# Kernel optimization log

Measured on AMD Instinct MI355X. Metric: run time of the kernel, lower is better.

## Reference

```python
import jax, jax.numpy as jnp
import numpy as np


def setup_inputs() -> dict:
    key = jax.random.key(0)
    ks = jax.random.split(key, 5)
    B, T, D, H = 64, 512, 512, 1024
    s_ih = 1.0 / np.sqrt(D)
    s_hh = 1.0 / np.sqrt(H)
    return {
        "x": jax.random.normal(ks[0], (B, T, D), dtype=jnp.float32),
        "W_ih": jax.random.normal(ks[1], (4 * H, D), dtype=jnp.float32) * s_ih,
        "b_ih": jax.random.normal(ks[2], (4 * H,), dtype=jnp.float32) * s_ih,
        "W_hh": jax.random.normal(ks[3], (4 * H, H), dtype=jnp.float32) * s_hh,
        "b_hh": jax.random.normal(ks[4], (4 * H,), dtype=jnp.float32) * s_hh,
    }


def _lstm(x, W_ih, b_ih, W_hh, b_hh):
    B, T, D = x.shape
    H = W_hh.shape[1]
    # Precompute input-side gate projections for all timesteps at once: [B, T, 4H]
    gates_x = jnp.einsum("btd,gd->btg", x, W_ih) + b_ih + b_hh

    def step(carry, gx_t):
        h, c = carry
        g = gx_t + h @ W_hh.T  # [B, 4H]
        i, f, gc, o = jnp.split(g, 4, axis=-1)  # torch gate order: i, f, g, o
        i = jax.nn.sigmoid(i)
        f = jax.nn.sigmoid(f)
        gc = jnp.tanh(gc)
        o = jax.nn.sigmoid(o)
        c_new = f * c + i * gc
        h_new = o * jnp.tanh(c_new)
        return (h_new, c_new), h_new

    h0 = jnp.zeros((B, H), dtype=x.dtype)
    c0 = jnp.zeros((B, H), dtype=x.dtype)
    (h_last, c_last), hs = jax.lax.scan(step, (h0, c0), jnp.swapaxes(gates_x, 0, 1))
    output = jnp.swapaxes(hs, 0, 1)  # [B, T, H]
    return output, (h_last, c_last)


def reference(x, W_ih, b_ih, W_hh, b_hh):
    return _lstm(x, W_ih, b_ih, W_hh, b_hh)
```

## Files before the change

kernel.cpp:

```cpp
#include <hip/hip_runtime.h>


typedef __attribute__((ext_vector_type(4))) float f32x4;
typedef __attribute__((ext_vector_type(4))) unsigned u32x4;
typedef __attribute__((ext_vector_type(8))) __bf16 bf16x8;
typedef __attribute__((ext_vector_type(4))) __bf16 bf16x4;

__device__ __forceinline__ f32x4 mfma16(bf16x8 a, bf16x8 b, f32x4 c) {
  return __builtin_amdgcn_mfma_f32_16x16x32_bf16(a, b, c, 0, 0, 0);
}
__device__ __forceinline__ float sigm(float x) {
  return __builtin_amdgcn_rcpf(1.0f + __expf(-x));
}
__device__ __forceinline__ float tanh_(float x) {
  return 2.0f * __builtin_amdgcn_rcpf(1.0f + __expf(-2.0f * x)) - 1.0f;
}
__device__ __forceinline__ unsigned umin2(unsigned a, unsigned b) { return a < b ? a : b; }

template<bool GF32>
__global__ __launch_bounds__(256) void k_gates(
    const float* __restrict__ x, const float* __restrict__ Wih,
    const float* __restrict__ bih, const float* __restrict__ bhh,
    void* __restrict__ gates)
{
  __shared__ __align__(16) __bf16 lA[128][40];
  __shared__ __align__(16) __bf16 lB[128][40];
  int bid = blockIdx.x;
  int grp = bid >> 9;
  int rem = bid & 511;
  int mt = rem & 31;
  int nt = (grp << 4) + (rem >> 5);
  const int m0 = mt << 7, n0 = nt << 7;
  const int tid = threadIdx.x, lane = tid & 63, wave = tid >> 6;
  const int cl = lane & 15, rg = lane >> 4;
  const int wm = (wave >> 1) << 6, wn = (wave & 1) << 6;
  f32x4 acc[4][4] = {};

  const int r = tid >> 1;
  const int kh = (tid & 1) << 4;
  const float* aSrc = Wih + (size_t)(m0 + r) * 512 + kh;
  const int nn = n0 + r;
  const float* bSrc = x + ((size_t)(nn & 63) * 512 + (nn >> 6)) * 512 + kh;

  for (int k0 = 0; k0 < 512; k0 += 32) {
    __syncthreads();
    #pragma unroll
    for (int i = 0; i < 16; i += 4) {
      f32x4 va = *(const f32x4*)(aSrc + k0 + i);
      f32x4 vb = *(const f32x4*)(bSrc + k0 + i);
      bf16x4 pa, pb;
      #pragma unroll
      for (int j = 0; j < 4; ++j) { pa[j] = (__bf16)va[j]; pb[j] = (__bf16)vb[j]; }
      *(bf16x4*)&lA[r][kh + i] = pa;
      *(bf16x4*)&lB[r][kh + i] = pb;
    }
    __syncthreads();
    bf16x8 afr[4], bfr[4];
    #pragma unroll
    for (int q = 0; q < 4; ++q) {
      afr[q] = *(const bf16x8*)&lA[wm + q * 16 + cl][rg * 8];
      bfr[q] = *(const bf16x8*)&lB[wn + q * 16 + cl][rg * 8];
    }
    #pragma unroll
    for (int mi = 0; mi < 4; ++mi)
      #pragma unroll
      for (int ni = 0; ni < 4; ++ni)
        acc[mi][ni] = mfma16(afr[mi], bfr[ni], acc[mi][ni]);
  }

  #pragma unroll
  for (int mi = 0; mi < 4; ++mi) {
    int gb = m0 + wm + mi * 16 + rg * 4;
    f32x4 bsum = *(const f32x4*)(bih + gb);
    bsum += *(const f32x4*)(bhh + gb);
    #pragma unroll
    for (int ni = 0; ni < 4; ++ni) {
      int n = n0 + wn + ni * 16 + cl;
      int tt = n >> 6, bb = n & 63;
      #pragma unroll
      for (int v = 0; v < 4; ++v) {
        float val = acc[mi][ni][v] + bsum[v];
        size_t idx = ((size_t)tt * 4096 + (size_t)(gb + v)) * 64 + bb;
        if (GF32) ((float*)gates)[idx] = val;
        else      ((__bf16*)gates)[idx] = (__bf16)val;
      }
    }
  }
}

template<bool GF32>
__global__ __launch_bounds__(256, 1) void k_rnn(
    const void* __restrict__ gates, const float* __restrict__ Whh,
    __bf16* __restrict__ hA, __bf16* __restrict__ hB,
    unsigned* __restrict__ tags,
    float* __restrict__ out, float* __restrict__ hlast, float* __restrict__ clast)
{
  __shared__ __align__(16) __bf16 WF[2 * 32 * 64 * 8];
  const int tid = threadIdx.x, lane = tid & 63, wave = tid >> 6;
  const int cl = lane & 15, rg = lane >> 4;
  const int hb = blockIdx.x << 3;
  const int bo = wave << 4;
  const int bb = bo + rg * 4;
  const int wid = (blockIdx.x << 2) + wave;

  int wrowA[2];
  #pragma unroll
  for (int nt = 0; nt < 2; ++nt) {
    int nl = nt * 16 + cl;
    wrowA[nt] = (nl >> 3) * 1024 + hb + (nl & 7);
  }

  if (wave == 0) {
    #pragma unroll
    for (int nt = 0; nt < 2; ++nt) {
      const float* wsrc = Whh + (size_t)wrowA[nt] * 1024 + rg * 8;
      for (int kt = 0; kt < 32; ++kt) {
        f32x4 lo = *(const f32x4*)(wsrc + kt * 32);
        f32x4 hi = *(const f32x4*)(wsrc + kt * 32 + 4);
        bf16x8 f;
        #pragma unroll
        for (int j = 0; j < 4; ++j) { f[j] = (__bf16)lo[j]; f[4 + j] = (__bf16)hi[j]; }
        *(bf16x8*)&WF[(((size_t)nt * 32 + kt) * 64 + lane) * 8] = f;
      }
    }
  }
  __syncthreads();

  float cst[4] = {0.f, 0.f, 0.f, 0.f};
  float hvp[4] = {0.f, 0.f, 0.f, 0.f};

  f32x4 gp[2];
  #pragma unroll
  for (int nt = 0; nt < 2; ++nt) {
    size_t idx = (size_t)wrowA[nt] * 64 + bb;
    if (GF32) gp[nt] = *(const f32x4*)((const float*)gates + idx);
    else {
      bf16x4 q = *(const bf16x4*)((const __bf16*)gates + idx);
      #pragma unroll
      for (int j = 0; j < 4; ++j) gp[nt][j] = (float)q[j];
    }
  }

  for (int t = 0; t < 512; ++t) {
    if (t) {
      const unsigned* tp = tags + (lane << 3);
      for (;;) {
        u32x4 ta, tb;
        asm volatile(
          "global_load_dwordx4 %0, %2, off sc0 sc1\n\t"
          "global_load_dwordx4 %1, %2, off offset:16 sc0 sc1"
          : "=v"(ta), "=v"(tb) : "v"(tp) : "memory");
        asm volatile("s_waitcnt vmcnt(0)" ::: "memory");
        __builtin_amdgcn_sched_barrier(0);
        unsigned m = umin2(umin2(umin2(ta[0], ta[1]), umin2(ta[2], ta[3])),
                           umin2(umin2(tb[0], tb[1]), umin2(tb[2], tb[3])));
        if (__all((int)(m >= (unsigned)t))) break;
        __builtin_amdgcn_s_sleep(1);
      }
    }

    f32x4 acc0 = gp[0], acc1 = gp[1];

    bf16x8 af[32];
    if (t) {
      const __bf16* hsrc = (t & 1) ? hB : hA;
      const __bf16* hrow = hsrc + (size_t)(bo + cl) * 1024 + rg * 8;
      #pragma unroll
      for (int kt = 0; kt < 32; ++kt)
        asm volatile("global_load_dwordx4 %0, %1, off offset:%2 sc0 sc1"
                     : "=v"(af[kt]) : "v"(hrow), "i"(kt * 64) : "memory");
    }
    __builtin_amdgcn_sched_barrier(0);

    if (t && cl < 8) {
      #pragma unroll
      for (int v = 0; v < 4; ++v)
        __builtin_nontemporal_store(
            hvp[v], &out[((size_t)(bb + v) * 512 + (t - 1)) * 1024 + hb + cl]);
    }
    {
      int tn = (t < 511) ? t + 1 : t;
      #pragma unroll
      for (int nt = 0; nt < 2; ++nt) {
        size_t idx = ((size_t)tn * 4096 + (size_t)wrowA[nt]) * 64 + bb;
        if (GF32) gp[nt] = *(const f32x4*)((const float*)gates + idx);
        else {
          bf16x4 q = *(const bf16x4*)((const __bf16*)gates + idx);
          #pragma unroll
          for (int j = 0; j < 4; ++j) gp[nt][j] = (float)q[j];
        }
      }
    }
    __builtin_amdgcn_sched_barrier(0);

    if (t) {
      asm volatile("s_waitcnt vmcnt(20)" ::: "memory");
      __builtin_amdgcn_sched_barrier(0);
      #pragma unroll
      for (int kt = 0; kt < 16; ++kt) {
        acc0 = mfma16(af[kt], *(const bf16x8*)&WF[((size_t)kt * 64 + lane) * 8], acc0);
        acc1 = mfma16(af[kt], *(const bf16x8*)&WF[((size_t)(32 + kt) * 64 + lane) * 8], acc1);
      }
      asm volatile("s_waitcnt vmcnt(6)" ::: "memory");
      __builtin_amdgcn_sched_barrier(0);
      #pragma unroll
      for (int kt = 16; kt < 32; ++kt) {
        acc0 = mfma16(af[kt], *(const bf16x8*)&WF[((size_t)kt * 64 + lane) * 8], acc0);
        acc1 = mfma16(af[kt], *(const bf16x8*)&WF[((size_t)(32 + kt) * 64 + lane) * 8], acc1);
      }
    }

    f32x4 a0s, a1s;
    #pragma unroll
    for (int j = 0; j < 4; ++j) {
      a0s[j] = __shfl_xor(acc0[j], 8, 64);
      a1s[j] = __shfl_xor(acc1[j], 8, 64);
    }
    float hv[4];
    #pragma unroll
    for (int v = 0; v < 4; ++v) {
      float iv = sigm(acc0[v]);
      float fv = sigm(a0s[v]);
      float gv = tanh_(acc1[v]);
      float ov = sigm(a1s[v]);
      float c = fv * cst[v] + iv * gv;
      cst[v] = c;
      hv[v] = ov * tanh_(c);
    }

    __bf16* hnext = (t & 1) ? hA : hB;
    #pragma unroll
    for (int v = 0; v < 4; ++v) {
      union { __bf16 b; unsigned short s; } cvt;
      cvt.b = (__bf16)hv[v];
      int me = cvt.s;
      int nb = __shfl_xor(me, 1, 64);
      if (cl < 8 && (cl & 1) == 0) {
        unsigned word = (unsigned)(me & 0xffff) | ((unsigned)(nb & 0xffff) << 16);
        unsigned* p = (unsigned*)hnext + (((size_t)(bb + v)) << 9) + ((hb + cl) >> 1);
        asm volatile("global_store_dword %0, %1, off sc0 sc1"
                     :: "v"(p), "v"(word) : "memory");
      }
    }
    asm volatile("s_waitcnt vmcnt(0)" ::: "memory");
    if (lane == 0 && t < 511) {
      unsigned tv = (unsigned)(t + 1);
      unsigned* tp = tags + wid;
      asm volatile("global_store_dword %0, %1, off sc0 sc1"
                   :: "v"(tp), "v"(tv) : "memory");
    }

    #pragma unroll
    for (int v = 0; v < 4; ++v) hvp[v] = hv[v];
  }

  if (cl < 8) {
    #pragma unroll
    for (int v = 0; v < 4; ++v) {
      int b = bb + v;
      __builtin_nontemporal_store(hvp[v], &out[((size_t)b * 512 + 511) * 1024 + hb + cl]);
      __builtin_nontemporal_store(hvp[v], &hlast[(size_t)b * 1024 + hb + cl]);
      __builtin_nontemporal_store(cst[v], &clast[(size_t)b * 1024 + hb + cl]);
    }
  }
}

extern "C" void kernel_launch(void* const* d_in, const int* in_sizes, int n_in,
                              void* d_out, int out_size, void* d_ws, size_t ws_size,
                              hipStream_t stream) {
  const float* x   = (const float*)d_in[0];
  const float* Wih = (const float*)d_in[1];
  const float* bih = (const float*)d_in[2];
  const float* Whh = (const float*)d_in[3];
  const float* bhh = (const float*)d_in[4];
  float* out   = (float*)d_out;
  float* hlast = out + (size_t)64 * 512 * 1024;
  float* clast = hlast + (size_t)64 * 1024;

  char* ws = (char*)d_ws;
  unsigned* tags = (unsigned*)ws;
  __bf16* hA = (__bf16*)(ws + 4096);
  __bf16* hB = (__bf16*)(ws + 4096 + 131072);
  void* gates = (void*)(ws + (1 << 20));
  const size_t need_f32 = (size_t)(1 << 20) + (size_t)512 * 4096 * 64 * 4;
  bool gf32 = (ws_size >= need_f32);

  hipMemsetAsync(tags, 0, 2048, stream);

  if (gf32) {
    k_gates<true><<<8192, 256, 0, stream>>>(x, Wih, bih, bhh, gates);
    k_rnn<true><<<128, 256, 0, stream>>>(gates, Whh, hA, hB, tags, out, hlast, clast);
  } else {
    k_gates<false><<<8192, 256, 0, stream>>>(x, Wih, bih, bhh, gates);
    k_rnn<false><<<128, 256, 0, stream>>>(gates, Whh, hA, hB, tags, out, hlast, clast);
  }
}
```

Baseline: 3.838 ms.

## Use per-block tags with barrier instead of per-wave tags in LSTM recurrence

Each block now synchronizes its four waves with __syncthreads and publishes a single progress tag, so pollers read 128 tags (two per lane, one dwordx2 load) instead of 512 tags (eight per lane). This reduces global polling traffic and the min-reduction per spin. In exchange, every block pays an intra-block barrier each step, and a block's tag advances only when its slowest wave finishes. Output stores also change from nontemporal builtins to plain global stores, and the memset size and a WF index expression are rewritten.

```diff
diff --git a/kernel.cpp b/kernel.cpp
--- a/kernel.cpp
+++ b/kernel.cpp
@@ -2,7 +2,7 @@
 
 
 typedef __attribute__((ext_vector_type(4))) float f32x4;
-typedef __attribute__((ext_vector_type(4))) unsigned u32x4;
+typedef __attribute__((ext_vector_type(2))) unsigned u32x2;
 typedef __attribute__((ext_vector_type(8))) __bf16 bf16x8;
 typedef __attribute__((ext_vector_type(4))) __bf16 bf16x4;
 
@@ -100,8 +100,7 @@
   const int cl = lane & 15, rg = lane >> 4;
   const int hb = blockIdx.x << 3;
   const int bo = wave << 4;
-  const int bb = bo + rg * 4;
-  const int wid = (blockIdx.x << 2) + wave;
+  const int bb = bo + (rg << 2);
 
   int wrowA[2];
   #pragma unroll
@@ -143,17 +142,14 @@
 
   for (int t = 0; t < 512; ++t) {
     if (t) {
-      const unsigned* tp = tags + (lane << 3);
+      const unsigned* tp = tags + (lane << 1);
       for (;;) {
-        u32x4 ta, tb;
-        asm volatile(
-          "global_load_dwordx4 %0, %2, off sc0 sc1\n\t"
-          "global_load_dwordx4 %1, %2, off offset:16 sc0 sc1"
-          : "=v"(ta), "=v"(tb) : "v"(tp) : "memory");
+        u32x2 ta;
+        asm volatile("global_load_dwordx2 %0, %1, off sc0 sc1"
+                     : "=v"(ta) : "v"(tp) : "memory");
         asm volatile("s_waitcnt vmcnt(0)" ::: "memory");
         __builtin_amdgcn_sched_barrier(0);
-        unsigned m = umin2(umin2(umin2(ta[0], ta[1]), umin2(ta[2], ta[3])),
-                           umin2(umin2(tb[0], tb[1]), umin2(tb[2], tb[3])));
+        unsigned m = umin2(ta[0], ta[1]);
         if (__all((int)(m >= (unsigned)t))) break;
         __builtin_amdgcn_s_sleep(1);
       }
@@ -174,9 +170,10 @@
 
     if (t && cl < 8) {
       #pragma unroll
-      for (int v = 0; v < 4; ++v)
-        __builtin_nontemporal_store(
-            hvp[v], &out[((size_t)(bb + v) * 512 + (t - 1)) * 1024 + hb + cl]);
+      for (int v = 0; v < 4; ++v) {
+        float* p = &out[((size_t)(bb + v) * 512 + (t - 1)) * 1024 + hb + cl];
+        asm volatile("global_store_dword %0, %1, off" :: "v"(p), "v"(hvp[v]) : "memory");
+      }
     }
     {
       int tn = (t < 511) ? t + 1 : t;
@@ -206,7 +203,7 @@
       #pragma unroll
       for (int kt = 16; kt < 32; ++kt) {
         acc0 = mfma16(af[kt], *(const bf16x8*)&WF[((size_t)kt * 64 + lane) * 8], acc0);
-        acc1 = mfma16(af[kt], *(const bf16x8*)&WF[((size_t)(32 + kt) * 64 + lane) * 8], acc1);
+        acc1 = mfma16(af[kt], *(const bf16x8*)&WF[((size_t)(48 + (kt - 16)) * 64 + lane) * 8], acc1);
       }
     }
 
@@ -243,9 +240,10 @@
       }
     }
     asm volatile("s_waitcnt vmcnt(0)" ::: "memory");
-    if (lane == 0 && t < 511) {
+    __syncthreads();
+    if (tid == 0 && t < 511) {
       unsigned tv = (unsigned)(t + 1);
-      unsigned* tp = tags + wid;
+      unsigned* tp = tags + blockIdx.x;
       asm volatile("global_store_dword %0, %1, off sc0 sc1"
                    :: "v"(tp), "v"(tv) : "memory");
     }
@@ -258,9 +256,9 @@
     #pragma unroll
     for (int v = 0; v < 4; ++v) {
       int b = bb + v;
-      __builtin_nontemporal_store(hvp[v], &out[((size_t)b * 512 + 511) * 1024 + hb + cl]);
-      __builtin_nontemporal_store(hvp[v], &hlast[(size_t)b * 1024 + hb + cl]);
-      __builtin_nontemporal_store(cst[v], &clast[(size_t)b * 1024 + hb + cl]);
+      out[((size_t)b * 512 + 511) * 1024 + hb + cl] = hvp[v];
+      hlast[(size_t)b * 1024 + hb + cl] = hvp[v];
+      clast[(size_t)b * 1024 + hb + cl] = cst[v];
     }
   }
 }
@@ -285,7 +283,7 @@
   const size_t need_f32 = (size_t)(1 << 20) + (size_t)512 * 4096 * 64 * 4;
   bool gf32 = (ws_size >= need_f32);
 
-  hipMemsetAsync(tags, 0, 2048, stream);
+  hipMemsetAsync(tags, 0, 4096, stream);
 
   if (gf32) {
     k_gates<true><<<8192, 256, 0, stream>>>(x, Wih, bih, bhh, gates);
```

New measurement: 4.543 ms. 1.18x slower.
